# Performance work log

Measured on AMD Instinct MI355X. Metric: run time of the kernel, lower is better.

The kernel has to match this reference:

```python
import jax, jax.numpy as jnp
import numpy as np

S, B, C = 14, 2, 20          # grid size, boxes per cell, classes
LAMBDA_COORD, LAMBDA_NOOBJ = 5.0, 0.5
NCH = 5 * B + C              # 30 channels


def setup_inputs() -> dict:
    key = jax.random.key(0)
    k1, k2, k3 = jax.random.split(key, 3)
    Nb = 4096
    # positive values: loss takes sqrt(w), sqrt(h)
    pred = jax.random.uniform(k1, (Nb, S, S, NCH), dtype=jnp.float32, minval=0.05, maxval=1.0)
    target = jax.random.uniform(k2, (Nb, S, S, NCH), dtype=jnp.float32, minval=0.05, maxval=1.0)
    # binarize conf channels so coord (conf>0) / noobj (conf==0) partition the cells
    objf = (jax.random.uniform(k3, (Nb, S, S)) < 0.3).astype(jnp.float32)
    for b in range(B):
        target = target.at[..., 4 + 5 * b].set(objf)
    return {"pred_tensor": pred, "target_tensor": target}


def _to_xyxy(box):
    # box [..., 5] (or [..., B, 5]): cell-relative x,y and global w,h -> corners
    xy = box[..., :2] / S
    half = 0.5 * box[..., 2:4]
    return jnp.concatenate([xy - half, xy + half], axis=-1)


def reference(pred_tensor, target_tensor):
    pred, target = pred_tensor, target_tensor
    obj = (target[..., 4] > 0).astype(pred.dtype)      # [Nb,S,S]
    noobj = (target[..., 4] == 0).astype(pred.dtype)   # [Nb,S,S]

    pb = pred[..., :5 * B].reshape(pred.shape[:3] + (B, 5))     # [Nb,S,S,B,5]
    tb = target[..., :5 * B].reshape(target.shape[:3] + (B, 5))  # [Nb,S,S,B,5]

    # no-object confidence loss: conf channel of every box slot in noobj cells
    loss_noobj = jnp.sum(noobj[..., None] * (pb[..., 4] - tb[..., 4]) ** 2)

    # IoU of each of B predicted boxes vs the (first) target box of the cell
    pxy = _to_xyxy(pb)                        # [Nb,S,S,B,4]
    txy = _to_xyxy(tb[..., 0, :])[..., None, :]  # [Nb,S,S,1,4]
    lt = jnp.maximum(pxy[..., :2], txy[..., :2])
    rb = jnp.minimum(pxy[..., 2:], txy[..., 2:])
    wh = jnp.clip(rb - lt, 0.0)
    inter = wh[..., 0] * wh[..., 1]           # [Nb,S,S,B]
    area_p = (pxy[..., 2] - pxy[..., 0]) * (pxy[..., 3] - pxy[..., 1])
    area_t = (txy[..., 2] - txy[..., 0]) * (txy[..., 3] - txy[..., 1])
    iou = inter / (area_p + area_t - inter)

    max_iou = jax.lax.stop_gradient(jnp.max(iou, axis=-1))  # torch uses .data (detach)
    r = jnp.argmax(iou, axis=-1)              # responsible box index [Nb,S,S]

    pr = jnp.take_along_axis(pb, r[..., None, None], axis=3)[..., 0, :]  # [Nb,S,S,5]
    tr = jnp.take_along_axis(tb, r[..., None, None], axis=3)[..., 0, :]

    m = obj
    loss_xy = jnp.sum(m[..., None] * (pr[..., :2] - tr[..., :2]) ** 2)
    # guard sqrt in masked-out cells (values there don't matter)
    safe_pwh = jnp.where(m[..., None] > 0, pr[..., 2:4], 1.0)
    safe_twh = jnp.where(m[..., None] > 0, tr[..., 2:4], 1.0)
    loss_wh = jnp.sum(m[..., None] * (jnp.sqrt(safe_pwh) - jnp.sqrt(safe_twh)) ** 2)
    loss_obj = jnp.sum(m * (pr[..., 4] - max_iou) ** 2)
    loss_class = jnp.sum(m[..., None] * (pred[..., 5 * B:] - target[..., 5 * B:]) ** 2)

    loss = LAMBDA_COORD * (loss_xy + loss_wh) + loss_obj + LAMBDA_NOOBJ * loss_noobj + loss_class
    return loss / pred.shape[0]
```

## Files before the change

kernel.cpp:

```cpp
#include <hip/hip_runtime.h>


#define NB 4096
#define NCELL (NB * 14 * 14)
#define NCH 30
#define WAVE_CELLS 128
#define NBLOCKS (NCELL / WAVE_CELLS)
#define SEG 1024

#define GLOBAL_AS __attribute__((address_space(1)))
#define LDS_AS    __attribute__((address_space(3)))

__device__ __forceinline__ void async16(const char* g, char* l) {
    __builtin_amdgcn_global_load_lds((const GLOBAL_AS void*)g, (LDS_AS void*)l,
                                     16, 0, 0);
}

__device__ __forceinline__ float cell_loss_lds(const float* __restrict__ pl,
                                               const float* __restrict__ tl)
{
    const float2* p2 = (const float2*)pl;
    const float2* t2 = (const float2*)tl;

    float p[10], t[10];
#pragma unroll
    for (int i = 0; i < 5; ++i) {
        float2 a = p2[i]; p[2 * i] = a.x; p[2 * i + 1] = a.y;
        float2 b = t2[i]; t[2 * i] = b.x; t[2 * i + 1] = b.y;
    }

    const float t4 = t[4];
    const bool obj = (t4 > 0.0f);

    float dn0 = p[4] - t[4];
    float dn1 = p[9] - t[9];
    float noobj_l = (t4 == 0.0f) ? (dn0 * dn0 + dn1 * dn1) : 0.0f;

    const float invS = 1.0f / 14.0f;
    float tcx = t[0] * invS, tcy = t[1] * invS;
    float tx1 = tcx - 0.5f * t[2], ty1 = tcy - 0.5f * t[3];
    float tx2 = tcx + 0.5f * t[2], ty2 = tcy + 0.5f * t[3];
    float area_t = (tx2 - tx1) * (ty2 - ty1);

    float iou[2];
#pragma unroll
    for (int b = 0; b < 2; ++b) {
        const float* pb = p + 5 * b;
        float cx = pb[0] * invS, cy = pb[1] * invS;
        float x1 = cx - 0.5f * pb[2], y1 = cy - 0.5f * pb[3];
        float x2 = cx + 0.5f * pb[2], y2 = cy + 0.5f * pb[3];
        float lx = fmaxf(x1, tx1), ly = fmaxf(y1, ty1);
        float rx = fminf(x2, tx2), ry = fminf(y2, ty2);
        float wx = fmaxf(rx - lx, 0.0f), wy = fmaxf(ry - ly, 0.0f);
        float inter = wx * wy;
        float area_p = (x2 - x1) * (y2 - y1);
        iou[b] = inter / (area_p + area_t - inter);
    }

    const bool r = (iou[1] > iou[0]);
    float max_iou = fmaxf(iou[0], iou[1]);

    float pr0 = r ? p[5] : p[0], tr0 = r ? t[5] : t[0];
    float pr1 = r ? p[6] : p[1], tr1 = r ? t[6] : t[1];
    float pr2 = r ? p[7] : p[2], tr2 = r ? t[7] : t[2];
    float pr3 = r ? p[8] : p[3], tr3 = r ? t[8] : t[3];
    float pr4 = r ? p[9] : p[4];

    float lcls = 0.0f;
#pragma unroll
    for (int i = 5; i < 15; ++i) {
        float2 a = p2[i];
        float2 b = t2[i];
        float d0 = a.x - b.x, d1 = a.y - b.y;
        lcls += d0 * d0 + d1 * d1;
    }

    float obj_l = 0.0f;
    if (obj) {
        float dx = pr0 - tr0, dy = pr1 - tr1;
        float lxy = dx * dx + dy * dy;
        float dw = sqrtf(pr2) - sqrtf(tr2);
        float dh = sqrtf(pr3) - sqrtf(tr3);
        float lwh = dw * dw + dh * dh;
        float dob = pr4 - max_iou;
        float lob = dob * dob;
        obj_l = 5.0f * (lxy + lwh) + lob + lcls;
    }
    return obj_l + 0.5f * noobj_l;
}

__global__ __launch_bounds__(64) void yolo_loss_partial(
    const float* __restrict__ pred, const float* __restrict__ target,
    float* __restrict__ partial)
{
    __shared__ __align__(16) float pbuf[WAVE_CELLS * NCH];
    __shared__ __align__(16) float tbuf[WAVE_CELLS * NCH];

    const int lane = threadIdx.x;
    const size_t base = (size_t)blockIdx.x * WAVE_CELLS * NCH;
    const char* gp = (const char*)(pred + base);
    const char* gt = (const char*)(target + base);
    char* lp = (char*)pbuf;
    char* lt = (char*)tbuf;
    const int lo = lane * 16;

#pragma unroll
    for (int r = 0; r < 15; ++r) {
        async16(gp + r * SEG + lo, lp + r * SEG + lo);
        async16(gt + r * SEG + lo, lt + r * SEG + lo);
    }

    asm volatile("s_waitcnt vmcnt(14)" ::: "memory");
    __builtin_amdgcn_sched_barrier(0);
    float acc = cell_loss_lds(pbuf + lane * NCH, tbuf + lane * NCH);

    asm volatile("s_waitcnt vmcnt(0)" ::: "memory");
    __builtin_amdgcn_sched_barrier(0);
    acc += cell_loss_lds(pbuf + (64 + lane) * NCH, tbuf + (64 + lane) * NCH);

    float v = acc;
#pragma unroll
    for (int off = 32; off > 0; off >>= 1)
        v += __shfl_down(v, off, 64);
    if (lane == 0)
        partial[blockIdx.x] = v;
}

__global__ __launch_bounds__(256) void yolo_loss_finalize(
    const float* __restrict__ partial, float* __restrict__ out)
{
    double s = 0.0;
    for (int i = threadIdx.x; i < NBLOCKS; i += 256)
        s += (double)partial[i];

    __shared__ double sh[256];
    sh[threadIdx.x] = s;
    __syncthreads();
#pragma unroll
    for (int step = 128; step > 0; step >>= 1) {
        if (threadIdx.x < step) sh[threadIdx.x] += sh[threadIdx.x + step];
        __syncthreads();
    }
    if (threadIdx.x == 0)
        out[0] = (float)(sh[0] / (double)NB);
}

extern "C" void kernel_launch(void* const* d_in, const int* in_sizes, int n_in,
                              void* d_out, int out_size, void* d_ws, size_t ws_size,
                              hipStream_t stream) {
    const float* pred = (const float*)d_in[0];
    const float* target = (const float*)d_in[1];
    float* out = (float*)d_out;
    float* partial = (float*)d_ws;

    yolo_loss_partial<<<NBLOCKS, 64, 0, stream>>>(pred, target, partial);
    yolo_loss_finalize<<<1, 256, 0, stream>>>(partial, out);
}
```

Baseline: 211.4 us.

## Halve cells per wave and split load/compute into two half-wave phases

Each block now handles 64 cells instead of 128, which doubles the grid and halves LDS per block. The 7680-byte region per tensor is loaded as seven 16-byte rounds plus two 4-byte tail loads. The first 32 lanes start computing after the first four rounds have landed, and the other 32 lanes compute after all loads finish. The aim is more waves in flight to hide memory latency, at the cost of more partials, more small 4-byte loads, and half the lanes idling in each compute phase.

```diff
diff --git a/kernel.cpp b/kernel.cpp
--- a/kernel.cpp
+++ b/kernel.cpp
@@ -4,9 +4,9 @@
 #define NB 4096
 #define NCELL (NB * 14 * 14)
 #define NCH 30
-#define WAVE_CELLS 128
+#define WAVE_CELLS 64
 #define NBLOCKS (NCELL / WAVE_CELLS)
-#define SEG 1024
+#define REGION_B (WAVE_CELLS * NCH * 4)
 
 #define GLOBAL_AS __attribute__((address_space(1)))
 #define LDS_AS    __attribute__((address_space(3)))
@@ -14,6 +14,10 @@
 __device__ __forceinline__ void async16(const char* g, char* l) {
     __builtin_amdgcn_global_load_lds((const GLOBAL_AS void*)g, (LDS_AS void*)l,
                                      16, 0, 0);
+}
+__device__ __forceinline__ void async4(const char* g, char* l) {
+    __builtin_amdgcn_global_load_lds((const GLOBAL_AS void*)g, (LDS_AS void*)l,
+                                     4, 0, 0);
 }
 
 __device__ __forceinline__ float cell_loss_lds(const float* __restrict__ pl,
@@ -93,30 +97,45 @@
     const float* __restrict__ pred, const float* __restrict__ target,
     float* __restrict__ partial)
 {
-    __shared__ __align__(16) float pbuf[WAVE_CELLS * NCH];
-    __shared__ __align__(16) float tbuf[WAVE_CELLS * NCH];
+    __shared__ __align__(16) float pbuf[REGION_B / 4];
+    __shared__ __align__(16) float tbuf[REGION_B / 4];
 
     const int lane = threadIdx.x;
-    const size_t base = (size_t)blockIdx.x * WAVE_CELLS * NCH;
-    const char* gp = (const char*)(pred + base);
-    const char* gt = (const char*)(target + base);
+    const size_t base = (size_t)blockIdx.x * REGION_B;
+    const char* gp = (const char*)pred + base;
+    const char* gt = (const char*)target + base;
     char* lp = (char*)pbuf;
     char* lt = (char*)tbuf;
-    const int lo = lane * 16;
+
+    const int o16 = lane * 16;
+    const int o4 = 7168 + lane * 4;
 
 #pragma unroll
-    for (int r = 0; r < 15; ++r) {
-        async16(gp + r * SEG + lo, lp + r * SEG + lo);
-        async16(gt + r * SEG + lo, lt + r * SEG + lo);
+    for (int r = 0; r < 4; ++r) {
+        async16(gp + r * 1024 + o16, lp + r * 1024 + o16);
+        async16(gt + r * 1024 + o16, lt + r * 1024 + o16);
     }
+    __builtin_amdgcn_sched_barrier(0);
+#pragma unroll
+    for (int r = 4; r < 7; ++r) {
+        async16(gp + r * 1024 + o16, lp + r * 1024 + o16);
+        async16(gt + r * 1024 + o16, lt + r * 1024 + o16);
+    }
+    async4(gp + o4, lp + o4);
+    async4(gt + o4, lt + o4);
+    async4(gp + o4 + 256, lp + o4 + 256);
+    async4(gt + o4 + 256, lt + o4 + 256);
 
-    asm volatile("s_waitcnt vmcnt(14)" ::: "memory");
+    float acc = 0.0f;
+    asm volatile("s_waitcnt vmcnt(10)" ::: "memory");
     __builtin_amdgcn_sched_barrier(0);
-    float acc = cell_loss_lds(pbuf + lane * NCH, tbuf + lane * NCH);
+    if (lane < 32)
+        acc = cell_loss_lds(pbuf + lane * NCH, tbuf + lane * NCH);
 
     asm volatile("s_waitcnt vmcnt(0)" ::: "memory");
     __builtin_amdgcn_sched_barrier(0);
-    acc += cell_loss_lds(pbuf + (64 + lane) * NCH, tbuf + (64 + lane) * NCH);
+    if (lane >= 32)
+        acc = cell_loss_lds(pbuf + lane * NCH, tbuf + lane * NCH);
 
     float v = acc;
 #pragma unroll
```

Result: slower. 216.4 us (+2.4%).
